# Performance work log

Measured on AMD Instinct MI355X. Metric: run time of the kernel, lower is better.

## Reference

```python
import jax, jax.numpy as jnp
import numpy as np

# Inner-product factors for Cl(1,3) (Minkowski metric diag(+,-,-,-)).
# For blade e_b, <~e_b e_b>_0 = product of the metric signs of its constituent vectors.
# Blade order: [1, e0,e1,e2,e3, e01,e02,e03,e12,e13,e23, e012,e013,e023,e123, e0123]
_IPF = jnp.array([1, 1, -1, -1, -1, -1, -1, -1, 1, 1, 1, 1, 1, 1, -1, -1], dtype=jnp.float32)

B, H, N, CMV, CS = 4, 8, 2048, 8, 16


def setup_inputs() -> dict:
    key = jax.random.key(0)
    ks = jax.random.split(key, 6)
    f = lambda k, s: jax.random.normal(k, s, dtype=jnp.float32)
    return {
        "q_mv": f(ks[0], (B, H, N, CMV, 16)),
        "k_mv": f(ks[1], (B, H, N, CMV, 16)),
        "v_mv": f(ks[2], (B, H, N, CMV, 16)),
        "q_s": f(ks[3], (B, H, N, CS)),
        "k_s": f(ks[4], (B, H, N, CS)),
        "v_s": f(ks[5], (B, H, N, CS)),
    }


def reference(q_mv, k_mv, v_mv, q_s, k_s, v_s):
    b, h, n, cmv, _ = q_mv.shape
    cs = q_s.shape[-1]
    cmv_out = v_mv.shape[-2]
    cs_out = v_s.shape[-1]
    # GA inner product on mv part = euclidean dot after applying metric factors to queries
    q = jnp.concatenate([(q_mv * _IPF).reshape(b, h, n, cmv * 16), q_s], axis=-1)
    k = jnp.concatenate([k_mv.reshape(b, h, n, cmv * 16), k_s], axis=-1)
    v = jnp.concatenate([v_mv.reshape(b, h, n, cmv_out * 16), v_s], axis=-1)
    scale = 1.0 / np.sqrt(q.shape[-1]).astype(np.float32)  # torch SDPA default scale
    scores = jnp.einsum("bhid,bhjd->bhij", q, k) * scale  # [B,H,N,N]
    attn = jax.nn.softmax(scores, axis=-1)
    out = jnp.einsum("bhij,bhjd->bhid", attn, v)
    out_mv = out[..., : cmv_out * 16].reshape(b, h, n, cmv_out, 16)
    out_s = out[..., cmv_out * 16 : cmv_out * 16 + cs_out]
    return out_mv, out_s
```

## Files before the change

### kernel.cpp

```cpp
#include <hip/hip_runtime.h>
#include <cstdint>
#include <math.h>


#define BH    32
#define N_    2048
#define DMV   128
#define DS    16
#define D_    144
#define BM    256
#define BN    64
#define NKIT  (N_ / BN)
#define KSTR  152
#define VSTR  72
#define SVROWS 160
#define KCHUNKS (BN * KSTR / 8)
#define VCHUNKS (D_ * VSTR / 8)
#define KP_BYTES ((size_t)BH * N_ * KSTR * 2)
#define QSCALE 0.12022458674074693f
#define KPACK_BLOCKS (BH * N_ * 19 / 256)
#define TSTR  156

typedef __bf16 bf16_8 __attribute__((ext_vector_type(8)));
typedef __bf16 bf16_4 __attribute__((ext_vector_type(4)));
typedef __bf16 bf16_2 __attribute__((ext_vector_type(2)));
typedef float  f32x4  __attribute__((ext_vector_type(4)));
typedef float  f32x16 __attribute__((ext_vector_type(16)));

#define GLOAD_LDS16(g, l)                                                     \
  __builtin_amdgcn_global_load_lds(                                           \
      (const __attribute__((address_space(1))) void*)(g),                     \
      (__attribute__((address_space(3))) void*)(l), 16, 0, 0)

__device__ __forceinline__ f32x16 mfma32(bf16_8 a, bf16_8 b, f32x16 c) {
  return __builtin_amdgcn_mfma_f32_32x32x16_bf16(a, b, c, 0, 0, 0);
}

__device__ __forceinline__ bf16_4 cvt4(f32x4 x) {
  bf16_4 w; w[0]=(__bf16)x[0]; w[1]=(__bf16)x[1]; w[2]=(__bf16)x[2]; w[3]=(__bf16)x[3];
  return w;
}

__global__ __launch_bounds__(256)
void pack_kv(const float* __restrict__ kmv, const float* __restrict__ ks_,
             const float* __restrict__ vmv, const float* __restrict__ vs,
             __bf16* __restrict__ kp, __bf16* __restrict__ vt) {
  __shared__ __align__(16) __bf16 sT[64 * TSTR];
  const int t = threadIdx.x;
  const int b = blockIdx.x;
  if (b < KPACK_BLOCKS) {
    const unsigned g = b * 256u + t;
    const unsigned row = g / 19u, seg = g - row * 19u;
    bf16_8 o;
    if (seg < 16) {
      const f32x4* p = (const f32x4*)(kmv + (size_t)row * DMV + seg * 8);
      f32x4 a = p[0], bb = p[1];
#pragma unroll
      for (int j = 0; j < 8; ++j) o[j] = (__bf16)((j < 4) ? a[j] : bb[j - 4]);
    } else if (seg < 18) {
      const f32x4* p = (const f32x4*)(ks_ + (size_t)row * DS + (seg - 16) * 8);
      f32x4 a = p[0], bb = p[1];
#pragma unroll
      for (int j = 0; j < 8; ++j) o[j] = (__bf16)((j < 4) ? a[j] : bb[j - 4]);
    } else {
#pragma unroll
      for (int j = 0; j < 8; ++j) o[j] = (__bf16)0.0f;
    }
    *(bf16_8*)(kp + (size_t)row * KSTR + seg * 8) = o;
    return;
  }
  const int tile = b - KPACK_BLOCKS;
  const int n = t >> 2, c = t & 3;
  const float* mv = vmv + (size_t)(tile * 64 + n) * DMV;
  const float* sv = vs  + (size_t)(tile * 64 + n) * DS;
  __bf16* row = &sT[n * TSTR];
  if (c < 3) {
#pragma unroll
    for (int i = 0; i < 9; ++i)
      *(bf16_4*)&row[c * 36 + 4 * i] = cvt4(*(const f32x4*)(mv + c * 36 + 4 * i));
  } else {
#pragma unroll
    for (int i = 0; i < 5; ++i)
      *(bf16_4*)&row[108 + 4 * i] = cvt4(*(const f32x4*)(mv + 108 + 4 * i));
#pragma unroll
    for (int i = 0; i < 4; ++i)
      *(bf16_4*)&row[128 + 4 * i] = cvt4(*(const f32x4*)(sv + 4 * i));
  }
  __syncthreads();
  __bf16* vtt = vt + (size_t)tile * (D_ * VSTR);
#pragma unroll
  for (int k = 0; k < 18; ++k) {
    int idx = t + 256 * k;
    int d = idx >> 5, j = idx & 31;
    bf16_2 p; p[0] = sT[(2 * j) * TSTR + d]; p[1] = sT[(2 * j + 1) * TSTR + d];
    *(bf16_2*)&vtt[d * VSTR + 2 * j] = p;
  }
}

__device__ __forceinline__ bf16_8 load_q_frag(const float* qmv_row, const float* qs_row, int k0) {
  bf16_8 f;
  if (k0 < DMV) {
    const f32x4* p = (const f32x4*)(qmv_row + k0);
    f32x4 a = p[0], b = p[1];
    int hi8 = k0 & 8;
#pragma unroll
    for (int j = 0; j < 8; ++j) {
      float v = (j < 4) ? a[j] : b[j - 4];
      bool pos = hi8 ? (j < 6) : (j < 2);
      f[j] = (__bf16)(v * (pos ? QSCALE : -QSCALE));
    }
  } else {
    const f32x4* p = (const f32x4*)(qs_row + (k0 - DMV));
    f32x4 a = p[0], b = p[1];
#pragma unroll
    for (int j = 0; j < 8; ++j) {
      float v = (j < 4) ? a[j] : b[j - 4];
      f[j] = (__bf16)(v * QSCALE);
    }
  }
  return f;
}

__global__ __launch_bounds__(512, 2)
void geo_attn_kernel(const float* __restrict__ q_mv, const float* __restrict__ q_s,
                     const __bf16* __restrict__ kp, const __bf16* __restrict__ vt,
                     float* __restrict__ out)
{
  __shared__ __align__(16) __bf16 sK[2][BN * KSTR];
  __shared__ __align__(16) __bf16 sVT[3][SVROWS * VSTR];

  const int tid  = threadIdx.x;
  const int lane = tid & 63;
  const int w    = tid >> 6;
  const int c32  = lane & 31;
  const int hi   = lane >> 5;
  const int flat = blockIdx.x;
  const int xcd  = flat & 7;
  const int jj   = flat >> 3;
  const int bh   = xcd * 4 + (jj & 3);
  const int qb   = jj >> 2;
  const int qbase = qb * BM;
  const size_t bh_n = (size_t)bh * N_;

  if (tid < 432) {
    int bb = tid / 144, cc = tid - bb * 144;
    f32x4 z = {0.f, 0.f, 0.f, 0.f};
    *(f32x4*)((char*)&sVT[bb][D_ * VSTR] + cc * 16) = z;
  }

  bf16_8 qf[9];
  {
    const int mrow = qbase + w * 32 + c32;
    const float* qmv_row = q_mv + (bh_n + mrow) * DMV;
    const float* qs_row  = q_s  + (bh_n + mrow) * DS;
#pragma unroll
    for (int ks = 0; ks < 9; ++ks)
      qf[ks] = load_q_frag(qmv_row, qs_row, ks * 16 + hi * 8);
  }

  f32x16 of[5];
#pragma unroll
  for (int dt = 0; dt < 5; ++dt)
#pragma unroll
    for (int r = 0; r < 16; ++r) of[dt][r] = 0.0f;
  float m_i = -INFINITY, l_i = 0.0f;

  const __bf16* kbase = kp + bh_n * KSTR;
  const __bf16* vbase = vt + (size_t)bh * NKIT * (D_ * VSTR);

  auto stageK = [&](int it, int bu) {
    const __bf16* kt = kbase + (size_t)(it * BN) * KSTR;
    __bf16* dK = &sK[bu][0];
    GLOAD_LDS16(kt + tid * 8, dK + tid * 8);
    GLOAD_LDS16(kt + (tid + 512) * 8, dK + (tid + 512) * 8);
    if (tid < KCHUNKS - 1024)
      GLOAD_LDS16(kt + (tid + 1024) * 8, dK + (tid + 1024) * 8);
  };
  auto stageV = [&](int it, int bu) {
    const __bf16* vtt = vbase + (size_t)it * (D_ * VSTR);
    __bf16* dV = &sVT[bu][0];
    GLOAD_LDS16(vtt + tid * 8, dV + tid * 8);
    GLOAD_LDS16(vtt + (tid + 512) * 8, dV + (tid + 512) * 8);
    if (tid < VCHUNKS - 1024)
      GLOAD_LDS16(vtt + (tid + 1024) * 8, dV + (tid + 1024) * 8);
  };

  auto qk = [&](int kb, f32x16 (&sn)[2]) {
#pragma unroll
    for (int nt = 0; nt < 2; ++nt)
#pragma unroll
      for (int r = 0; r < 16; ++r) sn[nt][r] = 0.0f;
    __builtin_amdgcn_s_setprio(1);
#pragma unroll
    for (int ks = 0; ks < 9; ++ks) {
      bf16_8 kb0 = *(const bf16_8*)&sK[kb][(c32)      * KSTR + ks * 16 + hi * 8];
      bf16_8 kb1 = *(const bf16_8*)&sK[kb][(32 + c32) * KSTR + ks * 16 + hi * 8];
      sn[0] = mfma32(kb0, qf[ks], sn[0]);
      sn[1] = mfma32(kb1, qf[ks], sn[1]);
    }
    __builtin_amdgcn_s_setprio(0);
  };

  auto body = [&](int t, f32x16 (&sfc)[2], f32x16 (&sfn)[2]) {
    __syncthreads();
    if (t + 2 < NKIT) {
      stageK(t + 2, t & 1);
      stageV(t + 2, (t + 2) % 3);
    }
    if (t + 1 < NKIT)
      qk((t + 1) & 1, sfn);

    float al = 1.0f, m_use;
    {
      float a[8];
#pragma unroll
      for (int r = 0; r < 8; ++r)
        a[r] = fmaxf(fmaxf(sfc[0][r], sfc[0][r + 8]), fmaxf(sfc[1][r], sfc[1][r + 8]));
      float mx = fmaxf(fmaxf(fmaxf(a[0], a[1]), fmaxf(a[2], a[3])),
                       fmaxf(fmaxf(a[4], a[5]), fmaxf(a[6], a[7])));
      mx = fmaxf(mx, __shfl_xor(mx, 32));

      if (__all(mx <= m_i + 8.0f)) {
        m_use = m_i;
      } else {
        float mnew = fmaxf(m_i, mx);
        al = __builtin_amdgcn_exp2f(m_i - mnew);
        m_i = mnew; m_use = mnew;
#pragma unroll
        for (int r = 0; r < 16; ++r) {
          float aa = __shfl(al, (r & 3) + 8 * (r >> 2) + 4 * hi);
#pragma unroll
          for (int dt = 0; dt < 5; ++dt) of[dt][r] *= aa;
        }
      }
#pragma unroll
      for (int nt = 0; nt < 2; ++nt)
#pragma unroll
        for (int r = 0; r < 16; ++r)
          sfc[nt][r] = __builtin_amdgcn_exp2f(sfc[nt][r] - m_use);
      float s8[8];
#pragma unroll
      for (int r = 0; r < 8; ++r)
        s8[r] = (sfc[0][r] + sfc[0][r + 8]) + (sfc[1][r] + sfc[1][r + 8]);
      float rs = ((s8[0] + s8[1]) + (s8[2] + s8[3])) + ((s8[4] + s8[5]) + (s8[6] + s8[7]));
      rs += __shfl_xor(rs, 32);
      l_i = l_i * al + rs;
    }

    const __bf16* sV = &sVT[t % 3][0];
#pragma unroll
    for (int ks = 0; ks < 4; ++ks) {
      const int nt = ks >> 1;
      const int Ra = 8 * (ks & 1);
      unsigned x0, x1, y0, y1;
      asm("v_cvt_pk_bf16_f32 %0, %1, %2" : "=v"(x0) : "v"(sfc[nt][Ra + 0]), "v"(sfc[nt][Ra + 1]));
      asm("v_cvt_pk_bf16_f32 %0, %1, %2" : "=v"(x1) : "v"(sfc[nt][Ra + 2]), "v"(sfc[nt][Ra + 3]));
      asm("v_cvt_pk_bf16_f32 %0, %1, %2" : "=v"(y0) : "v"(sfc[nt][Ra + 4]), "v"(sfc[nt][Ra + 5]));
      asm("v_cvt_pk_bf16_f32 %0, %1, %2" : "=v"(y1) : "v"(sfc[nt][Ra + 6]), "v"(sfc[nt][Ra + 7]));
      auto s0 = __builtin_amdgcn_permlane32_swap(x0, y0, false, false);
      auto s1 = __builtin_amdgcn_permlane32_swap(x1, y1, false, false);
      union { unsigned u[4]; bf16_8 v; } pu;
      pu.u[0] = s0[0]; pu.u[1] = s1[0]; pu.u[2] = s0[1]; pu.u[3] = s1[1];
      __builtin_amdgcn_s_setprio(1);
#pragma unroll
      for (int dt = 0; dt < 5; ++dt) {
        bf16_8 vb = *(const bf16_8*)&sV[(dt * 32 + c32) * VSTR + ks * 16 + hi * 8];
        of[dt] = mfma32(pu.v, vb, of[dt]);
      }
      __builtin_amdgcn_s_setprio(0);
    }
  };

  f32x16 sfA[2], sfB[2];
  stageK(0, 0); stageV(0, 0);
  __syncthreads();
  qk(0, sfA);
  stageK(1, 1); stageV(1, 1);

  for (int t2 = 0; t2 < NKIT; t2 += 2) {
    body(t2,     sfA, sfB);
    body(t2 + 1, sfB, sfA);
  }

  float* out_mv = out;
  float* out_s  = out + (size_t)BH * N_ * DMV;
#pragma unroll
  for (int r = 0; r < 16; ++r) {
    const int ml  = (r & 3) + 8 * (r >> 2) + 4 * hi;
    const float linv = __builtin_amdgcn_rcpf(__shfl(l_i, ml));
    const int row = qbase + w * 32 + ml;
#pragma unroll
    for (int dt = 0; dt < 4; ++dt)
      out_mv[(bh_n + row) * DMV + dt * 32 + c32] = of[dt][r] * linv;
    if (c32 < DS)
      out_s[(bh_n + row) * DS + c32] = of[4][r] * linv;
  }
}

extern "C" void kernel_launch(void* const* d_in, const int* in_sizes, int n_in,
                              void* d_out, int out_size, void* d_ws, size_t ws_size,
                              hipStream_t stream) {
  (void)in_sizes; (void)n_in; (void)out_size; (void)ws_size;
  const float* q_mv = (const float*)d_in[0];
  const float* k_mv = (const float*)d_in[1];
  const float* v_mv = (const float*)d_in[2];
  const float* q_s  = (const float*)d_in[3];
  const float* k_s  = (const float*)d_in[4];
  const float* v_s  = (const float*)d_in[5];
  float* out = (float*)d_out;

  __bf16* kp = (__bf16*)d_ws;
  __bf16* vt = (__bf16*)((char*)d_ws + KP_BYTES);

  pack_kv<<<KPACK_BLOCKS + BH * NKIT, 256, 0, stream>>>(k_mv, k_s, v_mv, v_s, kp, vt);

  geo_attn_kernel<<<dim3(256), 512, 0, stream>>>(q_mv, q_s, kp, vt, out);
}
```

Baseline: 241.9 us.

## Replace in-warp QK prefetch pipelining with a two-role warp ping-pong schedule

The main loop no longer computes QK for the next tile inside each warp while it runs softmax on the current one. Warps are now split into two roles: role 0 does QK, softmax and PV on tile t, while role 1 does softmax and PV on tile t-1 and then QK on tile t. The aim is to overlap MFMA and VALU work across warps instead of within a warp, with one barrier per iteration. Each warp now holds a single score accumulator, which lowers register pressure. The zero-padded V rows are dropped, so the unused output columns read whatever sits in the adjacent LDS, and the fused K/V pack kernel is split into two launches.

```diff
diff --git a/kernel.cpp b/kernel.cpp
--- a/kernel.cpp
+++ b/kernel.cpp
@@ -13,12 +13,10 @@
 #define NKIT  (N_ / BN)
 #define KSTR  152
 #define VSTR  72
-#define SVROWS 160
 #define KCHUNKS (BN * KSTR / 8)
 #define VCHUNKS (D_ * VSTR / 8)
 #define KP_BYTES ((size_t)BH * N_ * KSTR * 2)
 #define QSCALE 0.12022458674074693f
-#define KPACK_BLOCKS (BH * N_ * 19 / 256)
 #define TSTR  156
 
 typedef __bf16 bf16_8 __attribute__((ext_vector_type(8)));
@@ -42,34 +40,34 @@
 }
 
 __global__ __launch_bounds__(256)
-void pack_kv(const float* __restrict__ kmv, const float* __restrict__ ks_,
-             const float* __restrict__ vmv, const float* __restrict__ vs,
-             __bf16* __restrict__ kp, __bf16* __restrict__ vt) {
+void pack_k(const float* __restrict__ kmv, const float* __restrict__ ks_,
+            __bf16* __restrict__ kp) {
+  const unsigned g = blockIdx.x * 256u + threadIdx.x;
+  const unsigned row = g / 19u, seg = g - row * 19u;
+  bf16_8 o;
+  if (seg < 16) {
+    const f32x4* p = (const f32x4*)(kmv + (size_t)row * DMV + seg * 8);
+    f32x4 a = p[0], bb = p[1];
+#pragma unroll
+    for (int j = 0; j < 8; ++j) o[j] = (__bf16)((j < 4) ? a[j] : bb[j - 4]);
+  } else if (seg < 18) {
+    const f32x4* p = (const f32x4*)(ks_ + (size_t)row * DS + (seg - 16) * 8);
+    f32x4 a = p[0], bb = p[1];
+#pragma unroll
+    for (int j = 0; j < 8; ++j) o[j] = (__bf16)((j < 4) ? a[j] : bb[j - 4]);
+  } else {
+#pragma unroll
+    for (int j = 0; j < 8; ++j) o[j] = (__bf16)0.0f;
+  }
+  *(bf16_8*)(kp + (size_t)row * KSTR + seg * 8) = o;
+}
+
+__global__ __launch_bounds__(256)
+void pack_vt(const float* __restrict__ vmv, const float* __restrict__ vs,
+             __bf16* __restrict__ vt) {
   __shared__ __align__(16) __bf16 sT[64 * TSTR];
+  const int tile = blockIdx.x;
   const int t = threadIdx.x;
-  const int b = blockIdx.x;
-  if (b < KPACK_BLOCKS) {
-    const unsigned g = b * 256u + t;
-    const unsigned row = g / 19u, seg = g - row * 19u;
-    bf16_8 o;
-    if (seg < 16) {
-      const f32x4* p = (const f32x4*)(kmv + (size_t)row * DMV + seg * 8);
-      f32x4 a = p[0], bb = p[1];
-#pragma unroll
-      for (int j = 0; j < 8; ++j) o[j] = (__bf16)((j < 4) ? a[j] : bb[j - 4]);
-    } else if (seg < 18) {
-      const f32x4* p = (const f32x4*)(ks_ + (size_t)row * DS + (seg - 16) * 8);
-      f32x4 a = p[0], bb = p[1];
-#pragma unroll
-      for (int j = 0; j < 8; ++j) o[j] = (__bf16)((j < 4) ? a[j] : bb[j - 4]);
-    } else {
-#pragma unroll
-      for (int j = 0; j < 8; ++j) o[j] = (__bf16)0.0f;
-    }
-    *(bf16_8*)(kp + (size_t)row * KSTR + seg * 8) = o;
-    return;
-  }
-  const int tile = b - KPACK_BLOCKS;
   const int n = t >> 2, c = t & 3;
   const float* mv = vmv + (size_t)(tile * 64 + n) * DMV;
   const float* sv = vs  + (size_t)(tile * 64 + n) * DS;
@@ -126,12 +124,13 @@
                      const __bf16* __restrict__ kp, const __bf16* __restrict__ vt,
                      float* __restrict__ out)
 {
+  __shared__ __align__(16) __bf16 sVT[3][D_ * VSTR];
   __shared__ __align__(16) __bf16 sK[2][BN * KSTR];
-  __shared__ __align__(16) __bf16 sVT[3][SVROWS * VSTR];
 
   const int tid  = threadIdx.x;
   const int lane = tid & 63;
   const int w    = tid >> 6;
+  const int role = (w >> 2) & 1;
   const int c32  = lane & 31;
   const int hi   = lane >> 5;
   const int flat = blockIdx.x;
@@ -142,12 +141,6 @@
   const int qbase = qb * BM;
   const size_t bh_n = (size_t)bh * N_;
 
-  if (tid < 432) {
-    int bb = tid / 144, cc = tid - bb * 144;
-    f32x4 z = {0.f, 0.f, 0.f, 0.f};
-    *(f32x4*)((char*)&sVT[bb][D_ * VSTR] + cc * 16) = z;
-  }
-
   bf16_8 qf[9];
   {
     const int mrow = qbase + w * 32 + c32;
@@ -168,95 +161,87 @@
   const __bf16* kbase = kp + bh_n * KSTR;
   const __bf16* vbase = vt + (size_t)bh * NKIT * (D_ * VSTR);
 
-  auto stageK = [&](int it, int bu) {
+  auto stage = [&](int it) {
     const __bf16* kt = kbase + (size_t)(it * BN) * KSTR;
-    __bf16* dK = &sK[bu][0];
+    __bf16* dK = &sK[it & 1][0];
     GLOAD_LDS16(kt + tid * 8, dK + tid * 8);
     GLOAD_LDS16(kt + (tid + 512) * 8, dK + (tid + 512) * 8);
     if (tid < KCHUNKS - 1024)
       GLOAD_LDS16(kt + (tid + 1024) * 8, dK + (tid + 1024) * 8);
-  };
-  auto stageV = [&](int it, int bu) {
     const __bf16* vtt = vbase + (size_t)it * (D_ * VSTR);
-    __bf16* dV = &sVT[bu][0];
+    __bf16* dV = &sVT[it % 3][0];
     GLOAD_LDS16(vtt + tid * 8, dV + tid * 8);
     GLOAD_LDS16(vtt + (tid + 512) * 8, dV + (tid + 512) * 8);
     if (tid < VCHUNKS - 1024)
       GLOAD_LDS16(vtt + (tid + 1024) * 8, dV + (tid + 1024) * 8);
   };
 
-  auto qk = [&](int kb, f32x16 (&sn)[2]) {
+  f32x16 sf[2];
+  auto qk = [&](int t) {
+    const __bf16* sKt = &sK[t & 1][0];
 #pragma unroll
     for (int nt = 0; nt < 2; ++nt)
 #pragma unroll
-      for (int r = 0; r < 16; ++r) sn[nt][r] = 0.0f;
+      for (int r = 0; r < 16; ++r) sf[nt][r] = 0.0f;
     __builtin_amdgcn_s_setprio(1);
 #pragma unroll
     for (int ks = 0; ks < 9; ++ks) {
-      bf16_8 kb0 = *(const bf16_8*)&sK[kb][(c32)      * KSTR + ks * 16 + hi * 8];
-      bf16_8 kb1 = *(const bf16_8*)&sK[kb][(32 + c32) * KSTR + ks * 16 + hi * 8];
-      sn[0] = mfma32(kb0, qf[ks], sn[0]);
-      sn[1] = mfma32(kb1, qf[ks], sn[1]);
+      bf16_8 kb0 = *(const bf16_8*)&sKt[(c32)      * KSTR + ks * 16 + hi * 8];
+      bf16_8 kb1 = *(const bf16_8*)&sKt[(32 + c32) * KSTR + ks * 16 + hi * 8];
+      sf[0] = mfma32(kb0, qf[ks], sf[0]);
+      sf[1] = mfma32(kb1, qf[ks], sf[1]);
     }
     __builtin_amdgcn_s_setprio(0);
   };
 
-  auto body = [&](int t, f32x16 (&sfc)[2], f32x16 (&sfn)[2]) {
-    __syncthreads();
-    if (t + 2 < NKIT) {
-      stageK(t + 2, t & 1);
-      stageV(t + 2, (t + 2) % 3);
-    }
-    if (t + 1 < NKIT)
-      qk((t + 1) & 1, sfn);
-
+  auto sm = [&]() {
     float al = 1.0f, m_use;
-    {
-      float a[8];
-#pragma unroll
-      for (int r = 0; r < 8; ++r)
-        a[r] = fmaxf(fmaxf(sfc[0][r], sfc[0][r + 8]), fmaxf(sfc[1][r], sfc[1][r + 8]));
-      float mx = fmaxf(fmaxf(fmaxf(a[0], a[1]), fmaxf(a[2], a[3])),
-                       fmaxf(fmaxf(a[4], a[5]), fmaxf(a[6], a[7])));
-      mx = fmaxf(mx, __shfl_xor(mx, 32));
-
-      if (__all(mx <= m_i + 8.0f)) {
-        m_use = m_i;
-      } else {
-        float mnew = fmaxf(m_i, mx);
-        al = __builtin_amdgcn_exp2f(m_i - mnew);
-        m_i = mnew; m_use = mnew;
-#pragma unroll
-        for (int r = 0; r < 16; ++r) {
-          float aa = __shfl(al, (r & 3) + 8 * (r >> 2) + 4 * hi);
-#pragma unroll
-          for (int dt = 0; dt < 5; ++dt) of[dt][r] *= aa;
-        }
+    float a[8];
+#pragma unroll
+    for (int r = 0; r < 8; ++r)
+      a[r] = fmaxf(fmaxf(sf[0][r], sf[0][r + 8]), fmaxf(sf[1][r], sf[1][r + 8]));
+    float mx = fmaxf(fmaxf(fmaxf(a[0], a[1]), fmaxf(a[2], a[3])),
+                     fmaxf(fmaxf(a[4], a[5]), fmaxf(a[6], a[7])));
+    mx = fmaxf(mx, __shfl_xor(mx, 32));
+
+    if (__all(mx <= m_i + 8.0f)) {
+      m_use = m_i;
+    } else {
+      float mnew = fmaxf(m_i, mx);
+      al = __builtin_amdgcn_exp2f(m_i - mnew);
+      m_i = mnew; m_use = mnew;
+#pragma unroll
+      for (int r = 0; r < 16; ++r) {
+        float aa = __shfl(al, (r & 3) + 8 * (r >> 2) + 4 * hi);
+#pragma unroll
+        for (int dt = 0; dt < 5; ++dt) of[dt][r] *= aa;
       }
-#pragma unroll
-      for (int nt = 0; nt < 2; ++nt)
-#pragma unroll
-        for (int r = 0; r < 16; ++r)
-          sfc[nt][r] = __builtin_amdgcn_exp2f(sfc[nt][r] - m_use);
-      float s8[8];
-#pragma unroll
-      for (int r = 0; r < 8; ++r)
-        s8[r] = (sfc[0][r] + sfc[0][r + 8]) + (sfc[1][r] + sfc[1][r + 8]);
-      float rs = ((s8[0] + s8[1]) + (s8[2] + s8[3])) + ((s8[4] + s8[5]) + (s8[6] + s8[7]));
-      rs += __shfl_xor(rs, 32);
-      l_i = l_i * al + rs;
-    }
-
+    }
+#pragma unroll
+    for (int nt = 0; nt < 2; ++nt)
+#pragma unroll
+      for (int r = 0; r < 16; ++r)
+        sf[nt][r] = __builtin_amdgcn_exp2f(sf[nt][r] - m_use);
+    float s8[8];
+#pragma unroll
+    for (int r = 0; r < 8; ++r)
+      s8[r] = (sf[0][r] + sf[0][r + 8]) + (sf[1][r] + sf[1][r + 8]);
+    float rs = ((s8[0] + s8[1]) + (s8[2] + s8[3])) + ((s8[4] + s8[5]) + (s8[6] + s8[7]));
+    rs += __shfl_xor(rs, 32);
+    l_i = l_i * al + rs;
+  };
+
+  auto pv = [&](int t) {
     const __bf16* sV = &sVT[t % 3][0];
 #pragma unroll
     for (int ks = 0; ks < 4; ++ks) {
       const int nt = ks >> 1;
       const int Ra = 8 * (ks & 1);
       unsigned x0, x1, y0, y1;
-      asm("v_cvt_pk_bf16_f32 %0, %1, %2" : "=v"(x0) : "v"(sfc[nt][Ra + 0]), "v"(sfc[nt][Ra + 1]));
-      asm("v_cvt_pk_bf16_f32 %0, %1, %2" : "=v"(x1) : "v"(sfc[nt][Ra + 2]), "v"(sfc[nt][Ra + 3]));
-      asm("v_cvt_pk_bf16_f32 %0, %1, %2" : "=v"(y0) : "v"(sfc[nt][Ra + 4]), "v"(sfc[nt][Ra + 5]));
-      asm("v_cvt_pk_bf16_f32 %0, %1, %2" : "=v"(y1) : "v"(sfc[nt][Ra + 6]), "v"(sfc[nt][Ra + 7]));
+      asm("v_cvt_pk_bf16_f32 %0, %1, %2" : "=v"(x0) : "v"(sf[nt][Ra + 0]), "v"(sf[nt][Ra + 1]));
+      asm("v_cvt_pk_bf16_f32 %0, %1, %2" : "=v"(x1) : "v"(sf[nt][Ra + 2]), "v"(sf[nt][Ra + 3]));
+      asm("v_cvt_pk_bf16_f32 %0, %1, %2" : "=v"(y0) : "v"(sf[nt][Ra + 4]), "v"(sf[nt][Ra + 5]));
+      asm("v_cvt_pk_bf16_f32 %0, %1, %2" : "=v"(y1) : "v"(sf[nt][Ra + 6]), "v"(sf[nt][Ra + 7]));
       auto s0 = __builtin_amdgcn_permlane32_swap(x0, y0, false, false);
       auto s1 = __builtin_amdgcn_permlane32_swap(x1, y1, false, false);
       union { unsigned u[4]; bf16_8 v; } pu;
@@ -271,16 +256,20 @@
     }
   };
 
-  f32x16 sfA[2], sfB[2];
-  stageK(0, 0); stageV(0, 0);
+  stage(0);
   __syncthreads();
-  qk(0, sfA);
-  stageK(1, 1); stageV(1, 1);
-
-  for (int t2 = 0; t2 < NKIT; t2 += 2) {
-    body(t2,     sfA, sfB);
-    body(t2 + 1, sfB, sfA);
-  }
+
+  for (int t = 0; t < NKIT; ++t) {
+    if (t + 1 < NKIT) stage(t + 1);
+    if (role == 0) {
+      qk(t); sm(); pv(t);
+    } else {
+      if (t > 0) { sm(); pv(t - 1); }
+      qk(t);
+    }
+    __syncthreads();
+  }
+  if (role == 1) { sm(); pv(NKIT - 1); }
 
   float* out_mv = out;
   float* out_s  = out + (size_t)BH * N_ * DMV;
@@ -312,7 +301,8 @@
   __bf16* kp = (__bf16*)d_ws;
   __bf16* vt = (__bf16*)((char*)d_ws + KP_BYTES);
 
-  pack_kv<<<KPACK_BLOCKS + BH * NKIT, 256, 0, stream>>>(k_mv, k_s, v_mv, v_s, kp, vt);
+  pack_k<<<(BH * N_ * 19) / 256, 256, 0, stream>>>(k_mv, k_s, kp);
+  pack_vt<<<BH * NKIT, 256, 0, stream>>>(v_mv, v_s, vt);
 
   geo_attn_kernel<<<dim3(256), 512, 0, stream>>>(q_mv, q_s, kp, vt, out);
 }
```

New measurement: 241.7 us. About the same (-0.1%).
